# Kernel tuning notes

Hardware: AMD Instinct MI355X
Metric: run time of the kernel (lower is better)

Reference implementation:

```python
import jax, jax.numpy as jnp
import numpy as np

NEG_INF = -1e20

def setup_inputs() -> dict:
    key = jax.random.key(0)
    kq, kk, kv, km = jax.random.split(key, 4)
    B, S, H, D = 2, 2048, 16, 64
    queries = jax.random.normal(kq, (B, S, H, D), dtype=jnp.float32)
    keys = jax.random.normal(kk, (B, S, H, D), dtype=jnp.float32)
    values = jax.random.normal(kv, (B, S, H, D), dtype=jnp.float32)
    mask = jax.random.randint(km, (B, 1, 1, S), 0, 2, dtype=jnp.int32)
    return {"queries": queries, "keys": keys, "values": values, "mask": mask}

def reference(queries, keys, values, mask):
    # scores: [B, H, Q, K]
    dk = keys.shape[-1]
    scores = jnp.einsum('bqhd,bkhd->bhqk', queries, keys) / jnp.sqrt(jnp.asarray(dk, queries.dtype))
    scores = jnp.where(mask == 0, jnp.asarray(NEG_INF, scores.dtype), scores)
    attn = jax.nn.softmax(scores, axis=-1)
    # dropout p=0.0 (eval): identity
    out = jnp.einsum('bhqv,bvhd->bqhd', attn, values)
    return out
```

## Files before the change

kernel.cpp:

```cpp
#include <hip/hip_runtime.h>
#include <hip/hip_bf16.h>

#define S_LEN 2048
#define NH 16
#define HD 64

typedef __attribute__((ext_vector_type(8))) __bf16 bf16x8;
typedef __attribute__((ext_vector_type(16))) float f32x16;

#define QSCALE 0.1803368801111204f

static __device__ __forceinline__ ushort f2bf(float f) {
    unsigned int u = __float_as_uint(f);
    u += 0x7fffu + ((u >> 16) & 1u);
    return (ushort)(u >> 16);
}

static __device__ __forceinline__ void gload16(const void* g, void* l) {
    __builtin_amdgcn_global_load_lds(
        (const __attribute__((address_space(1))) unsigned int*)g,
        (__attribute__((address_space(3))) unsigned int*)l, 16, 0, 0);
}
static __device__ __forceinline__ void gload4(const void* g, void* l) {
    __builtin_amdgcn_global_load_lds(
        (const __attribute__((address_space(1))) unsigned int*)g,
        (__attribute__((address_space(3))) unsigned int*)l, 4, 0, 0);
}

static __device__ __forceinline__ unsigned cvtpk_bf16(float lo, float hi) {
    unsigned r;
    asm("v_cvt_pk_bf16_f32 %0, %1, %2" : "=v"(r) : "v"(lo), "v"(hi));
    return r;
}
static __device__ __forceinline__ float exp2_fast(float x) {
    float r;
    asm("v_exp_f32 %0, %1" : "=v"(r) : "v"(x));
    return r;
}

__global__ __launch_bounds__(256) void prep_k_kernel(const float* __restrict__ in,
                                                     ushort* __restrict__ out) {
    unsigned t = blockIdx.x * 256u + threadIdx.x;
    unsigned o = t & 7u;
    unsigned s = (t >> 3) & 2047u;
    unsigned bh = t >> 14;
    unsigned b = bh >> 4, h = bh & 15u;
    const float* src = in + (((size_t)(b * S_LEN) + s) * NH + h) * HD + o * 8;
    float4 x = *(const float4*)src;
    float4 y = *(const float4*)(src + 4);
    union { ushort u[8]; uint4 q; } fu;
    fu.u[0] = f2bf(x.x); fu.u[1] = f2bf(x.y); fu.u[2] = f2bf(x.z); fu.u[3] = f2bf(x.w);
    fu.u[4] = f2bf(y.x); fu.u[5] = f2bf(y.y); fu.u[6] = f2bf(y.z); fu.u[7] = f2bf(y.w);
    unsigned kt = s >> 6, kh = (s >> 5) & 1u, kl = s & 31u;
    unsigned dchunk = o >> 1, ho = o & 1u;
    size_t ci = (((size_t)(bh * 32u + kt) * 2u + kh) * 4u + dchunk) * 64u + kl + 32u * ho;
    *(uint4*)(out + ci * 8u) = fu.q;
}

__global__ __launch_bounds__(256) void prep_v_kernel(const float* __restrict__ in,
                                                     ushort* __restrict__ out) {
    __shared__ float T[64][68];
    const unsigned tid = threadIdx.x;
    const unsigned kt = blockIdx.x, bh = blockIdx.y;
    const unsigned b = bh >> 4, h = bh & 15u;
#pragma unroll
    for (int i = 0; i < 4; ++i) {
        unsigned idx = tid + i * 256u;
        unsigned sl = idx >> 4, d4 = (idx & 15u) * 4u;
        float4 v = *(const float4*)(in + (((size_t)(b * S_LEN) + kt * 64u + sl) * NH + h) * HD + d4);
        *(float4*)&T[sl][d4] = v;
    }
    __syncthreads();
#pragma unroll
    for (int it = 0; it < 2; ++it) {
        unsigned ct = tid + it * 256u;
        unsigned l = ct & 63u, sub = ct >> 6;
        unsigned nt = sub & 1u, c = (sub >> 1) & 1u, kh = sub >> 2;
        unsigned d = (l & 31u) + 32u * nt;
        unsigned kb = kh * 32u + c * 16u + (l >> 5) * 8u;
        union { ushort u[8]; uint4 q; } fu;
#pragma unroll
        for (int j = 0; j < 8; ++j) fu.u[j] = f2bf(T[kb + j][d]);
        *(uint4*)(out + ((size_t)(bh * 32u + kt) * 8u + sub) * 512u + l * 8u) = fu.q;
    }
}

struct TileMem {
    ushort K[2][2][4096];
    ushort V[2][2][4096];
    int    mb[2][2][64];
};
struct CombMem {
    float ob[4][32][64];
    float lsb[4][64];
    float rls[4][32];
};
union SMemU { TileMem s; CombMem c; };

__global__ __launch_bounds__(512, 4) void attn_kernel(const float* __restrict__ Qp,
                                                      const ushort* __restrict__ Kws,
                                                      const ushort* __restrict__ Vws,
                                                      const int* __restrict__ maskp,
                                                      float* __restrict__ outp) {
    __shared__ __align__(16) SMemU sm;

    const unsigned tid = threadIdx.x;
    const unsigned wid = tid >> 6;
    const unsigned lane = tid & 63u;
    const unsigned l31 = lane & 31u;
    const unsigned hi = lane >> 5;
    const unsigned qsub = wid & 3u;
    const unsigned kgrp = wid >> 2;

    const unsigned bh = blockIdx.y;
    const unsigned b = bh >> 4, h = bh & 15u;
    const unsigned q0 = blockIdx.x * 128u + qsub * 32u;

    bf16x8 qf[4];
    {
        const float* qb = Qp + (((size_t)(b * S_LEN) + q0 + l31) * NH + h) * HD + hi * 8u;
#pragma unroll
        for (int dc = 0; dc < 4; ++dc) {
            float4 x = *(const float4*)(qb + dc * 16);
            float4 y = *(const float4*)(qb + dc * 16 + 4);
            union { ushort u[8]; bf16x8 v; } fu;
            fu.u[0] = f2bf(x.x * QSCALE); fu.u[1] = f2bf(x.y * QSCALE);
            fu.u[2] = f2bf(x.z * QSCALE); fu.u[3] = f2bf(x.w * QSCALE);
            fu.u[4] = f2bf(y.x * QSCALE); fu.u[5] = f2bf(y.y * QSCALE);
            fu.u[6] = f2bf(y.z * QSCALE); fu.u[7] = f2bf(y.w * QSCALE);
            qf[dc] = fu.v;
        }
    }

    f32x16 oacc0 = {0,0,0,0,0,0,0,0,0,0,0,0,0,0,0,0};
    f32x16 oacc1 = {0,0,0,0,0,0,0,0,0,0,0,0,0,0,0,0};
    float ls0 = 0.f, ls1 = 0.f, ls2 = 0.f, ls3 = 0.f;

    const char* kgp = (const char*)Kws + (size_t)bh * 262144u
                    + ((size_t)kgrp * 131072u) + (2u * qsub) * 1024u + lane * 16u;
    const char* vgp = (const char*)Vws + (size_t)bh * 262144u
                    + ((size_t)kgrp * 131072u) + (2u * qsub) * 1024u + lane * 16u;
    const int* mgp = maskp + (size_t)b * S_LEN + kgrp * 1024u + lane;

    ushort* klb = &sm.s.K[kgrp][0][2u * qsub * 512u];
    ushort* vlb = &sm.s.V[kgrp][0][2u * qsub * 512u];
    int*    mlb = &sm.s.mb[kgrp][0][0];
    const ushort* krd = &sm.s.K[kgrp][0][0];
    const ushort* vrd = &sm.s.V[kgrp][0][0];

#define STAGE(I, PB) do {                                                      \
    const size_t toff = (size_t)(I) * 8192u;                                   \
    gload16(kgp + toff,          klb + (PB) * 4096u);                          \
    gload16(kgp + toff + 1024u,  klb + (PB) * 4096u + 512u);                   \
    gload16(vgp + toff,          vlb + (PB) * 4096u);                          \
    gload16(vgp + toff + 1024u,  vlb + (PB) * 4096u + 512u);                   \
    if (qsub == 0) gload4(mgp + (I) * 64, mlb + (PB) * 64u);                   \
  } while (0)

    STAGE(0, 0u);
    asm volatile("s_waitcnt vmcnt(0)" ::: "memory");
    __syncthreads();

    unsigned pb = 0;
    for (int i = 0; i < 16; ++i) {
        if (i < 15) STAGE(i + 1, pb ^ 1u);
        const ushort* kr = krd + pb * 4096u;
        const ushort* vr = vrd + pb * 4096u;
        const int*    mr = mlb + pb * 64u;

#pragma unroll
        for (int kh = 0; kh < 2; ++kh) {
            bf16x8 kf[4];
#pragma unroll
            for (int dc = 0; dc < 4; ++dc)
                kf[dc] = *(const bf16x8*)&kr[(kh * 4 + dc) * 512u + lane * 8u];

            f32x16 s = {0,0,0,0,0,0,0,0,0,0,0,0,0,0,0,0};
            __builtin_amdgcn_s_setprio(1);
#pragma unroll
            for (int dc = 0; dc < 4; ++dc)
                s = __builtin_amdgcn_mfma_f32_32x32x16_bf16(kf[dc], qf[dc], s, 0, 0, 0);
            __builtin_amdgcn_s_setprio(0);

            float p[16];
#pragma unroll
            for (int r1 = 0; r1 < 4; ++r1) {
                int mv[4];
                *(int4*)mv = *(const int4*)&mr[kh * 32 + r1 * 8 + hi * 4];
#pragma unroll
                for (int r0 = 0; r0 < 4; ++r0) {
                    const int reg = r1 * 4 + r0;
                    float t = mv[r0] ? s[reg] : -1e30f;
                    p[reg] = exp2_fast(t);
                }
                ls0 += p[r1 * 4 + 0]; ls1 += p[r1 * 4 + 1];
                ls2 += p[r1 * 4 + 2]; ls3 += p[r1 * 4 + 3];
            }

#pragma unroll
            for (int c = 0; c < 2; ++c) {
                unsigned x  = cvtpk_bf16(p[8 * c + 0], p[8 * c + 1]);
                unsigned x2 = cvtpk_bf16(p[8 * c + 2], p[8 * c + 3]);
                unsigned y  = cvtpk_bf16(p[8 * c + 4], p[8 * c + 5]);
                unsigned y2 = cvtpk_bf16(p[8 * c + 6], p[8 * c + 7]);
                unsigned xs  = (unsigned)__shfl_xor((int)x, 32);
                unsigned x2s = (unsigned)__shfl_xor((int)x2, 32);
                unsigned ys  = (unsigned)__shfl_xor((int)y, 32);
                unsigned y2s = (unsigned)__shfl_xor((int)y2, 32);
                union { unsigned w[4]; bf16x8 v; } pa;
                pa.w[0] = hi ? ys  : x;
                pa.w[1] = hi ? y2s : x2;
                pa.w[2] = hi ? y   : xs;
                pa.w[3] = hi ? y2  : x2s;
                bf16x8 vf0 = *(const bf16x8*)&vr[((kh * 2 + c) * 2 + 0) * 512u + lane * 8u];
                bf16x8 vf1 = *(const bf16x8*)&vr[((kh * 2 + c) * 2 + 1) * 512u + lane * 8u];
                __builtin_amdgcn_s_setprio(1);
                oacc0 = __builtin_amdgcn_mfma_f32_32x32x16_bf16(pa.v, vf0, oacc0, 0, 0, 0);
                oacc1 = __builtin_amdgcn_mfma_f32_32x32x16_bf16(pa.v, vf1, oacc1, 0, 0, 0);
                __builtin_amdgcn_s_setprio(0);
            }
        }
        asm volatile("s_waitcnt vmcnt(0)" ::: "memory");
        __syncthreads();
        pb ^= 1u;
    }
#undef STAGE

    float lsum = (ls0 + ls1) + (ls2 + ls3);
    lsum += __shfl_xor(lsum, 32);

    if (kgrp == 1) {
#pragma unroll
        for (int r = 0; r < 16; ++r) {
            sm.c.ob[qsub][r][lane]      = oacc0[r];
            sm.c.ob[qsub][16 + r][lane] = oacc1[r];
        }
        sm.c.lsb[qsub][lane] = lsum;
    }
    __syncthreads();
    if (kgrp == 0) {
        lsum += sm.c.lsb[qsub][lane];
#pragma unroll
        for (int r = 0; r < 16; ++r) {
            oacc0[r] += sm.c.ob[qsub][r][lane];
            oacc1[r] += sm.c.ob[qsub][16 + r][lane];
        }
        if (hi == 0) sm.c.rls[qsub][l31] = 1.0f / lsum;
#pragma unroll
        for (int r1 = 0; r1 < 4; ++r1) {
#pragma unroll
            for (int r0 = 0; r0 < 4; ++r0) {
                const int reg = r1 * 4 + r0;
                const unsigned q = r0 + 8u * r1 + 4u * hi;
                const float rr = sm.c.rls[qsub][q];
                float* ob = outp + (((size_t)(b * S_LEN) + q0 + q) * NH + h) * HD + l31;
                ob[0]  = oacc0[reg] * rr;
                ob[32] = oacc1[reg] * rr;
            }
        }
    }
}

extern "C" void kernel_launch(void* const* d_in, const int* in_sizes, int n_in,
                              void* d_out, int out_size, void* d_ws, size_t ws_size,
                              hipStream_t stream) {
    const float* Qp = (const float*)d_in[0];
    const float* Kp = (const float*)d_in[1];
    const float* Vp = (const float*)d_in[2];
    const int* maskp = (const int*)d_in[3];
    float* outp = (float*)d_out;

    ushort* Kws = (ushort*)d_ws;
    ushort* Vws = Kws + (size_t)2 * NH * S_LEN * HD;

    hipLaunchKernelGGL(prep_k_kernel, dim3(2048), dim3(256), 0, stream, Kp, Kws);
    hipLaunchKernelGGL(prep_v_kernel, dim3(32, 32), dim3(256), 0, stream, Vp, Vws);
    hipLaunchKernelGGL(attn_kernel, dim3(S_LEN / 128, 32), dim3(512), 0, stream,
                       Qp, Kws, Vws, maskp, outp);
}
```

Before: 68.18 us.

## Triple-buffer K in LDS, read V and mask from global, use permlane32 swap

```diff
diff --git a/kernel.cpp b/kernel.cpp
--- a/kernel.cpp
+++ b/kernel.cpp
@@ -20,11 +20,6 @@
     __builtin_amdgcn_global_load_lds(
         (const __attribute__((address_space(1))) unsigned int*)g,
         (__attribute__((address_space(3))) unsigned int*)l, 16, 0, 0);
-}
-static __device__ __forceinline__ void gload4(const void* g, void* l) {
-    __builtin_amdgcn_global_load_lds(
-        (const __attribute__((address_space(1))) unsigned int*)g,
-        (__attribute__((address_space(3))) unsigned int*)l, 4, 0, 0);
 }
 
 static __device__ __forceinline__ unsigned cvtpk_bf16(float lo, float hi) {
@@ -85,17 +80,15 @@
     }
 }
 
-struct TileMem {
-    ushort K[2][2][4096];
-    ushort V[2][2][4096];
-    int    mb[2][2][64];
-};
 struct CombMem {
     float ob[4][32][64];
     float lsb[4][64];
     float rls[4][32];
 };
-union SMemU { TileMem s; CombMem c; };
+union SMemU {
+    ushort K[2][3][4096];
+    CombMem c;
+};
 
 __global__ __launch_bounds__(512, 4) void attn_kernel(const float* __restrict__ Qp,
                                                       const ushort* __restrict__ Kws,
@@ -138,35 +131,32 @@
 
     const char* kgp = (const char*)Kws + (size_t)bh * 262144u
                     + ((size_t)kgrp * 131072u) + (2u * qsub) * 1024u + lane * 16u;
-    const char* vgp = (const char*)Vws + (size_t)bh * 262144u
-                    + ((size_t)kgrp * 131072u) + (2u * qsub) * 1024u + lane * 16u;
-    const int* mgp = maskp + (size_t)b * S_LEN + kgrp * 1024u + lane;
-
-    ushort* klb = &sm.s.K[kgrp][0][2u * qsub * 512u];
-    ushort* vlb = &sm.s.V[kgrp][0][2u * qsub * 512u];
-    int*    mlb = &sm.s.mb[kgrp][0][0];
-    const ushort* krd = &sm.s.K[kgrp][0][0];
-    const ushort* vrd = &sm.s.V[kgrp][0][0];
+    const ushort* vg = Vws + (size_t)bh * 131072u + (size_t)kgrp * 65536u + lane * 8u;
+    const int* mg = maskp + (size_t)b * S_LEN + kgrp * 1024u;
+
+    ushort* klb = &sm.K[kgrp][0][2u * qsub * 512u];
+    const ushort* krd = &sm.K[kgrp][0][0];
 
 #define STAGE(I, PB) do {                                                      \
     const size_t toff = (size_t)(I) * 8192u;                                   \
-    gload16(kgp + toff,          klb + (PB) * 4096u);                          \
-    gload16(kgp + toff + 1024u,  klb + (PB) * 4096u + 512u);                   \
-    gload16(vgp + toff,          vlb + (PB) * 4096u);                          \
-    gload16(vgp + toff + 1024u,  vlb + (PB) * 4096u + 512u);                   \
-    if (qsub == 0) gload4(mgp + (I) * 64, mlb + (PB) * 64u);                   \
+    gload16(kgp + toff,         klb + (PB) * 4096u);                           \
+    gload16(kgp + toff + 1024u, klb + (PB) * 4096u + 512u);                    \
   } while (0)
 
     STAGE(0, 0u);
-    asm volatile("s_waitcnt vmcnt(0)" ::: "memory");
-    __syncthreads();
-
-    unsigned pb = 0;
+    STAGE(1, 1u);
+    asm volatile("s_waitcnt vmcnt(2)" ::: "memory");
+    __builtin_amdgcn_s_barrier();
+
+    unsigned cur = 0u;
     for (int i = 0; i < 16; ++i) {
-        if (i < 15) STAGE(i + 1, pb ^ 1u);
-        const ushort* kr = krd + pb * 4096u;
-        const ushort* vr = vrd + pb * 4096u;
-        const int*    mr = mlb + pb * 64u;
+        if (i < 14) {
+            unsigned pb = (cur == 2u) ? 1u : ((cur == 1u) ? 0u : 2u);
+            STAGE(i + 2, pb);
+        }
+        const ushort* kr = krd + cur * 4096u;
+        const ushort* vt = vg + (unsigned)i * 4096u;
+        const int*    mt = mg + i * 64;
 
 #pragma unroll
         for (int kh = 0; kh < 2; ++kh) {
@@ -185,50 +175,44 @@
             float p[16];
 #pragma unroll
             for (int r1 = 0; r1 < 4; ++r1) {
-                int mv[4];
-                *(int4*)mv = *(const int4*)&mr[kh * 32 + r1 * 8 + hi * 4];
-#pragma unroll
-                for (int r0 = 0; r0 < 4; ++r0) {
-                    const int reg = r1 * 4 + r0;
-                    float t = mv[r0] ? s[reg] : -1e30f;
-                    p[reg] = exp2_fast(t);
-                }
+                int4 mv = *(const int4*)(mt + kh * 32 + r1 * 8 + hi * 4);
+                p[r1 * 4 + 0] = exp2_fast(mv.x ? s[r1 * 4 + 0] : -1e30f);
+                p[r1 * 4 + 1] = exp2_fast(mv.y ? s[r1 * 4 + 1] : -1e30f);
+                p[r1 * 4 + 2] = exp2_fast(mv.z ? s[r1 * 4 + 2] : -1e30f);
+                p[r1 * 4 + 3] = exp2_fast(mv.w ? s[r1 * 4 + 3] : -1e30f);
                 ls0 += p[r1 * 4 + 0]; ls1 += p[r1 * 4 + 1];
                 ls2 += p[r1 * 4 + 2]; ls3 += p[r1 * 4 + 3];
             }
 
 #pragma unroll
             for (int c = 0; c < 2; ++c) {
-                unsigned x  = cvtpk_bf16(p[8 * c + 0], p[8 * c + 1]);
-                unsigned x2 = cvtpk_bf16(p[8 * c + 2], p[8 * c + 3]);
-                unsigned y  = cvtpk_bf16(p[8 * c + 4], p[8 * c + 5]);
-                unsigned y2 = cvtpk_bf16(p[8 * c + 6], p[8 * c + 7]);
-                unsigned xs  = (unsigned)__shfl_xor((int)x, 32);
-                unsigned x2s = (unsigned)__shfl_xor((int)x2, 32);
-                unsigned ys  = (unsigned)__shfl_xor((int)y, 32);
-                unsigned y2s = (unsigned)__shfl_xor((int)y2, 32);
+                unsigned a0 = cvtpk_bf16(p[8 * c + 0], p[8 * c + 1]);
+                unsigned a1 = cvtpk_bf16(p[8 * c + 2], p[8 * c + 3]);
+                unsigned b0 = cvtpk_bf16(p[8 * c + 4], p[8 * c + 5]);
+                unsigned b1 = cvtpk_bf16(p[8 * c + 6], p[8 * c + 7]);
+                asm("v_permlane32_swap_b32 %0, %1" : "+v"(a0), "+v"(b0));
+                asm("v_permlane32_swap_b32 %0, %1" : "+v"(a1), "+v"(b1));
                 union { unsigned w[4]; bf16x8 v; } pa;
-                pa.w[0] = hi ? ys  : x;
-                pa.w[1] = hi ? y2s : x2;
-                pa.w[2] = hi ? y   : xs;
-                pa.w[3] = hi ? y2  : x2s;
-                bf16x8 vf0 = *(const bf16x8*)&vr[((kh * 2 + c) * 2 + 0) * 512u + lane * 8u];
-                bf16x8 vf1 = *(const bf16x8*)&vr[((kh * 2 + c) * 2 + 1) * 512u + lane * 8u];
+                pa.w[0] = a0; pa.w[1] = a1; pa.w[2] = b0; pa.w[3] = b1;
+                bf16x8 vf0 = *(const bf16x8*)(vt + ((kh * 2 + c) * 2 + 0) * 512u);
+                bf16x8 vf1 = *(const bf16x8*)(vt + ((kh * 2 + c) * 2 + 1) * 512u);
                 __builtin_amdgcn_s_setprio(1);
                 oacc0 = __builtin_amdgcn_mfma_f32_32x32x16_bf16(pa.v, vf0, oacc0, 0, 0, 0);
                 oacc1 = __builtin_amdgcn_mfma_f32_32x32x16_bf16(pa.v, vf1, oacc1, 0, 0, 0);
                 __builtin_amdgcn_s_setprio(0);
             }
         }
-        asm volatile("s_waitcnt vmcnt(0)" ::: "memory");
-        __syncthreads();
-        pb ^= 1u;
+
+        asm volatile("s_waitcnt vmcnt(2)" ::: "memory");
+        __builtin_amdgcn_s_barrier();
+        cur = (cur == 2u) ? 0u : cur + 1u;
     }
 #undef STAGE
 
     float lsum = (ls0 + ls1) + (ls2 + ls3);
     lsum += __shfl_xor(lsum, 32);
 
+    __syncthreads();
     if (kgrp == 1) {
 #pragma unroll
         for (int r = 0; r < 16; ++r) {
```

Result: slower. 83.04 us (+21.8%).
